# Kernel tuning notes

Measured on AMD Instinct MI355X. Metric: run time of the kernel, lower is better.

Reference implementation:

```python
import jax, jax.numpy as jnp
import numpy as np
import math

B, S, DIM, H, KVH = 2, 2048, 2048, 16, 4
HD = DIM // H          # 128
G = H // KVH           # 4 (GQA repeat factor)
NEG = -1e9             # fp32 additive mask value (matches torch path)


def _rotate_half(x):
    x1, x2 = jnp.split(x, 2, axis=-1)
    return jnp.concatenate([-x2, x1], axis=-1)


def setup_inputs() -> dict:
    key = jax.random.key(0)
    ks = jax.random.split(key, 8)
    hidden_states = jax.random.normal(ks[0], (B, S, DIM), jnp.float32)
    # standard RoPE tables [S, HD]
    inv_freq = 1.0 / (10000.0 ** (jnp.arange(0, HD, 2, dtype=jnp.float32) / HD))
    freqs = jnp.outer(jnp.arange(S, dtype=jnp.float32), inv_freq)
    emb = jnp.concatenate([freqs, freqs], axis=-1)
    position_cos = jnp.cos(emb)
    position_sin = jnp.sin(emb)
    alibi_bias = jax.random.normal(ks[1], (B, S, S), jnp.float32) * 0.01
    attention_mask = jnp.zeros((B, 1, 1, S), jnp.float32)
    sc = 0.02
    wq = jax.random.normal(ks[2], (DIM, DIM), jnp.float32) * sc
    wk = jax.random.normal(ks[3], (DIM, KVH * HD), jnp.float32) * sc
    wv = jax.random.normal(ks[4], (DIM, KVH * HD), jnp.float32) * sc
    wo = jax.random.normal(ks[5], (DIM, DIM), jnp.float32) * sc
    return {"hidden_states": hidden_states, "position_cos": position_cos,
            "position_sin": position_sin, "alibi_bias": alibi_bias,
            "attention_mask": attention_mask, "wq": wq, "wk": wk, "wv": wv, "wo": wo}


def reference(hidden_states, position_cos, position_sin, alibi_bias,
              attention_mask, wq, wk, wv, wo):
    b, s, d = hidden_states.shape
    # projections (weights stored as [in, out])
    q = (hidden_states @ wq).reshape(b, s, H, HD).transpose(0, 2, 1, 3)      # [B,H,S,HD]
    k = (hidden_states @ wk).reshape(b, s, KVH, HD).transpose(0, 2, 1, 3)    # [B,KVH,S,HD]
    v = (hidden_states @ wv).reshape(b, s, KVH, HD).transpose(0, 2, 1, 3)
    # RoPE
    cos = position_cos[None, None]  # [1,1,S,HD]
    sin = position_sin[None, None]
    q = q * cos + _rotate_half(q) * sin
    k = k * cos + _rotate_half(k) * sin
    # GQA repeat kv heads
    k = jnp.repeat(k, G, axis=1)   # [B,H,S,HD]
    v = jnp.repeat(v, G, axis=1)
    scores = jnp.einsum('bhqd,bhkd->bhqk', q, k) * (1.0 / math.sqrt(HD))
    causal = jnp.triu(jnp.full((s, s), NEG, jnp.float32), 1)
    scores = scores + causal + alibi_bias[:, None, :, :] + attention_mask
    attn = jax.nn.softmax(scores.astype(jnp.float32), axis=-1).astype(q.dtype)
    out = jnp.einsum('bhqk,bhkd->bhqd', attn, v)                              # [B,H,S,HD]
    out = out.transpose(0, 2, 1, 3).reshape(b, s, d)
    return out @ wo
```

## Files before the change

### kernel.cpp

```cpp
#include <hip/hip_runtime.h>
#include <hip/hip_bf16.h>

#define Bb   2
#define Ss   2048
#define Dd   2048
#define Hh   16
#define KVHh 4
#define HDd  128

typedef __bf16 bf16x8 __attribute__((ext_vector_type(8)));
typedef float f32x4 __attribute__((ext_vector_type(4)));

__device__ __forceinline__ unsigned short f2bf(float f) {
    unsigned u = __float_as_uint(f);
    unsigned r = (u + 0x7FFFu + ((u >> 16) & 1u)) >> 16;
    return (unsigned short)r;
}
__device__ __forceinline__ float bfu2f(unsigned short u) {
    return __uint_as_float(((unsigned)u) << 16);
}

#define GLOAD16(g, l) __builtin_amdgcn_global_load_lds( \
    (const __attribute__((address_space(1))) unsigned int*)(g), \
    (__attribute__((address_space(3))) unsigned int*)(l), 16, 0, 0)

__global__ __launch_bounds__(256)
void cast_bf16(const float* __restrict__ X, unsigned short* __restrict__ Y)
{
    int idx = blockIdx.x * 256 + threadIdx.x;
    float4 v = reinterpret_cast<const float4*>(X)[idx];
    ushort4 o;
    o.x = f2bf(v.x); o.y = f2bf(v.y); o.z = f2bf(v.z); o.w = f2bf(v.w);
    reinterpret_cast<ushort4*>(Y)[idx] = o;
}

__global__ __launch_bounds__(256)
void wt_cast(const float* __restrict__ W, unsigned short* __restrict__ WT,
             int K, int N)
{
    __shared__ float tile[32][33];
    int k0 = blockIdx.x * 32, n0 = blockIdx.y * 32;
    int tx = threadIdx.x & 31, ty = threadIdx.x >> 5;
    #pragma unroll
    for (int i = 0; i < 32; i += 8)
        tile[ty + i][tx] = W[(size_t)(k0 + ty + i) * N + n0 + tx];
    __syncthreads();
    #pragma unroll
    for (int i = 0; i < 32; i += 8)
        WT[(size_t)(n0 + ty + i) * K + k0 + tx] = f2bf(tile[tx][ty + i]);
}

template<bool BF16OUT>
__global__ __launch_bounds__(256)
void gemm_bt(const unsigned short* __restrict__ A,
             const unsigned short* __restrict__ BT,
             void* __restrict__ Cv, int M, int N, int K)
{
    __shared__ __align__(16) unsigned short sA[128 * 32];
    __shared__ __align__(16) unsigned short sB[128 * 32];
    const int tid  = threadIdx.x;
    const int wave = tid >> 6;
    const int lane = tid & 63;
    const int m    = lane & 15;
    const int quad = lane >> 4;
    const int wm   = wave >> 1, wn = wave & 1;
    const int m0   = blockIdx.y * 128, n0 = blockIdx.x * 128;

    const int srow = tid >> 2;
    const int skg  = (tid & 3) * 8;

    f32x4 acc[4][4];
    #pragma unroll
    for (int r = 0; r < 4; ++r)
        #pragma unroll
        for (int c = 0; c < 4; ++c) acc[r][c] = (f32x4){0.f, 0.f, 0.f, 0.f};

    const unsigned short* pa = A  + (size_t)(m0 + srow) * K + skg;
    const unsigned short* pb = BT + (size_t)(n0 + srow) * K + skg;
    unsigned short* la = &sA[wave * 16 * 32];
    unsigned short* lb = &sB[wave * 16 * 32];

    for (int k0 = 0; k0 < K; k0 += 32) {
        GLOAD16(pa + k0, la);
        GLOAD16(pa + (size_t)64 * K + k0, la + 64 * 32);
        GLOAD16(pb + k0, lb);
        GLOAD16(pb + (size_t)64 * K + k0, lb + 64 * 32);
        __syncthreads();
        bf16x8 af[4], bfr[4];
        #pragma unroll
        for (int r = 0; r < 4; ++r)
            af[r] = *reinterpret_cast<const bf16x8*>(
                &sA[(wm * 64 + r * 16 + m) * 32 + quad * 8]);
        #pragma unroll
        for (int c = 0; c < 4; ++c)
            bfr[c] = *reinterpret_cast<const bf16x8*>(
                &sB[(wn * 64 + c * 16 + m) * 32 + quad * 8]);
        #pragma unroll
        for (int r = 0; r < 4; ++r)
            #pragma unroll
            for (int c = 0; c < 4; ++c)
                acc[r][c] = __builtin_amdgcn_mfma_f32_16x16x32_bf16(
                    af[r], bfr[c], acc[r][c], 0, 0, 0);
        __syncthreads();
    }
    #pragma unroll
    for (int r = 0; r < 4; ++r)
        #pragma unroll
        for (int c = 0; c < 4; ++c)
            #pragma unroll
            for (int e = 0; e < 4; ++e) {
                size_t row = m0 + wm * 64 + r * 16 + quad * 4 + e;
                size_t col = n0 + wn * 64 + c * 16 + m;
                if (BF16OUT)
                    ((unsigned short*)Cv)[row * N + col] = f2bf(acc[r][c][e]);
                else
                    ((float*)Cv)[row * N + col] = acc[r][c][e];
            }
}

__global__ __launch_bounds__(256)
void rope_bf(unsigned short* __restrict__ X, const float* __restrict__ cosT,
             const float* __restrict__ sinT, int nhshift, int rowstride,
             float scale, int total)
{
    int idx = blockIdx.x * 256 + threadIdx.x;
    if (idx >= total) return;
    int i   = idx & 63;
    int rh  = idx >> 6;
    int row = rh >> nhshift;
    int h   = rh & ((1 << nhshift) - 1);
    int s   = row & (Ss - 1);
    unsigned short* xp = X + (size_t)row * rowstride + h * HDd;
    float x1 = bfu2f(xp[i]);
    float x2 = bfu2f(xp[i + 64]);
    float c1 = cosT[s * HDd + i];
    float c2 = cosT[s * HDd + i + 64];
    float s1 = sinT[s * HDd + i];
    float s2 = sinT[s * HDd + i + 64];
    xp[i]      = f2bf((x1 * c1 - x2 * s1) * scale);
    xp[i + 64] = f2bf((x2 * c2 + x1 * s2) * scale);
}

__global__ __launch_bounds__(256)
void vt_cast_bf(const unsigned short* __restrict__ KV,
                unsigned short* __restrict__ VT)
{
    __shared__ unsigned short tile[32][34];
    int st = blockIdx.x * 32, dt = blockIdx.y * 32;
    int bk = blockIdx.z;
    int b = bk >> 2, kvh = bk & 3;
    int tx = threadIdx.x & 31, ty = threadIdx.x >> 5;
    #pragma unroll
    for (int i = 0; i < 32; i += 8)
        tile[ty + i][tx] = KV[(size_t)(b * Ss + st + ty + i) * 1024 + 512 + kvh * HDd + dt + tx];
    __syncthreads();
    #pragma unroll
    for (int i = 0; i < 32; i += 8)
        VT[(((size_t)b * KVHh + kvh) * HDd + dt + ty + i) * Ss + st + tx] =
            tile[tx][ty + i];
}

__global__ __launch_bounds__(256, 2)
void flash_attn(const unsigned short* __restrict__ Qb,
                const unsigned short* __restrict__ KVb,
                const unsigned short* __restrict__ VT,
                const float* __restrict__ alibi,
                const float* __restrict__ amask,
                unsigned short* __restrict__ ctx)
{
    __shared__ __align__(16) unsigned short kbuf[2][32 * 128];
    __shared__ __align__(16) unsigned short vbuf[2][128 * 32];
    __shared__ unsigned short s_p[4][16][56];

    const int tid  = threadIdx.x;
    const int w    = tid >> 6;
    const int lane = tid & 63;
    const int m    = lane & 15;
    const int quad = lane >> 4;

    const int kvh = blockIdx.y;
    const int b   = blockIdx.z;
    const int h   = kvh * 4 + w;

    const unsigned short* vt0 = VT + ((size_t)b * KVHh + kvh) * HDd * Ss;
    const float* amrow = amask + (size_t)b * Ss;

    const int krow_s = tid >> 4;
    const int koff_b = ((tid & 15) * 16) ^ ((krow_s & 7) << 4);
    const int vrow_s = tid >> 2;
    const int vchk   = tid & 3;
    const int dstw   = w * 512;

    const unsigned short* kgbase = KVb + (size_t)b * Ss * 1024 + kvh * HDd;

    const int qts[2] = { (int)blockIdx.x, 127 - (int)blockIdx.x };

    #pragma unroll 1
    for (int pi = 0; pi < 2; ++pi) {
        const int q0 = qts[pi] * 16;

        bf16x8 qa[4];
        {
            const unsigned short* qrow = Qb + (size_t)(b * Ss + q0 + m) * Dd + h * HDd;
            #pragma unroll
            for (int c = 0; c < 4; ++c)
                qa[c] = *reinterpret_cast<const bf16x8*>(qrow + c * 32 + quad * 8);
        }

        f32x4 o[8];
        #pragma unroll
        for (int f = 0; f < 8; ++f) o[f] = (f32x4){0.f, 0.f, 0.f, 0.f};
        float lrow[4] = {0.f, 0.f, 0.f, 0.f};

        const float* arow = alibi + ((size_t)b * Ss + q0 + quad * 4) * Ss;
        const int ntiles = (q0 + 47) >> 5;

        {
            const unsigned short* kg = kgbase + (size_t)krow_s * 1024 + (koff_b >> 1);
            GLOAD16(kg,              &kbuf[0][dstw]);
            GLOAD16(kg + 16 * 1024,  &kbuf[0][2048 + dstw]);
            const unsigned short* vg = vt0 + (size_t)vrow_s * Ss + vchk * 8;
            GLOAD16(vg,              &vbuf[0][dstw]);
            GLOAD16(vg + 64 * Ss,    &vbuf[0][2048 + dstw]);
        }
        __syncthreads();

        #pragma unroll 1
        for (int kt = 0; kt < ntiles; ++kt) {
            const int k0  = kt * 32;
            const int cur = kt & 1;

            if (kt + 1 < ntiles) {
                const int kn = k0 + 32;
                const unsigned short* kg =
                    kgbase + (size_t)(kn + krow_s) * 1024 + (koff_b >> 1);
                GLOAD16(kg,              &kbuf[cur ^ 1][dstw]);
                GLOAD16(kg + 16 * 1024,  &kbuf[cur ^ 1][2048 + dstw]);
                const unsigned short* vg = vt0 + (size_t)vrow_s * Ss + kn + vchk * 8;
                GLOAD16(vg,              &vbuf[cur ^ 1][dstw]);
                GLOAD16(vg + 64 * Ss,    &vbuf[cur ^ 1][2048 + dstw]);
            }

            float al0[4], al1[4];
            #pragma unroll
            for (int r = 0; r < 4; ++r) {
                al0[r] = arow[(size_t)r * Ss + k0 + m];
                al1[r] = arow[(size_t)r * Ss + k0 + 16 + m];
            }
            const float am0 = amrow[k0 + m];
            const float am1 = amrow[k0 + 16 + m];

            const char* kb  = (const char*)&kbuf[cur][0];
            const char* vbp = (const char*)&vbuf[cur][0];
            const int  ksw  = (m & 7) << 4;
            bf16x8 kb0[4], kb1[4];
            #pragma unroll
            for (int c = 0; c < 4; ++c) {
                kb0[c] = *(const bf16x8*)(kb + m * 256        + ((c * 64 + quad * 16) ^ ksw));
                kb1[c] = *(const bf16x8*)(kb + (16 + m) * 256 + ((c * 64 + quad * 16) ^ ksw));
            }
            f32x4 s0 = {0.f, 0.f, 0.f, 0.f}, s1 = {0.f, 0.f, 0.f, 0.f};
            #pragma unroll
            for (int c = 0; c < 4; ++c) {
                s0 = __builtin_amdgcn_mfma_f32_16x16x32_bf16(qa[c], kb0[c], s0, 0, 0, 0);
                s1 = __builtin_amdgcn_mfma_f32_16x16x32_bf16(qa[c], kb1[c], s1, 0, 0, 0);
            }

            #pragma unroll
            for (int r = 0; r < 4; ++r) {
                const int qi = q0 + quad * 4 + r;
                float x0 = s0[r] + al0[r] + am0;
                float x1 = s1[r] + al1[r] + am1;
                x0 = (k0 + m      <= qi) ? x0 : -1e30f;
                x1 = (k0 + 16 + m <= qi) ? x1 : -1e30f;
                const float p0 = __expf(x0);
                const float p1 = __expf(x1);
                lrow[r] += p0 + p1;
                s_p[w][quad * 4 + r][m]      = f2bf(p0);
                s_p[w][quad * 4 + r][16 + m] = f2bf(p1);
            }
            __builtin_amdgcn_wave_barrier();
            const bf16x8 pa = *reinterpret_cast<const bf16x8*>(&s_p[w][m][quad * 8]);
            __builtin_amdgcn_wave_barrier();

            #pragma unroll
            for (int f = 0; f < 8; ++f) {
                const bf16x8 vb = *(const bf16x8*)(vbp + (f * 16 + m) * 64 + quad * 16);
                o[f] = __builtin_amdgcn_mfma_f32_16x16x32_bf16(pa, vb, o[f], 0, 0, 0);
            }

            __syncthreads();
        }

        float inv[4];
        #pragma unroll
        for (int r = 0; r < 4; ++r) {
            float l = lrow[r];
            l += __shfl_xor(l, 1, 64);
            l += __shfl_xor(l, 2, 64);
            l += __shfl_xor(l, 4, 64);
            l += __shfl_xor(l, 8, 64);
            inv[r] = 1.f / l;
        }
        #pragma unroll
        for (int f = 0; f < 8; ++f)
            #pragma unroll
            for (int r = 0; r < 4; ++r)
                ctx[(size_t)(b * Ss + q0 + quad * 4 + r) * Dd + h * HDd + f * 16 + m] =
                    f2bf(o[f][r] * inv[r]);
    }
}

extern "C" void kernel_launch(void* const* d_in, const int* in_sizes, int n_in,
                              void* d_out, int out_size, void* d_ws, size_t ws_size,
                              hipStream_t stream) {
    const float* hidden = (const float*)d_in[0];
    const float* cosT   = (const float*)d_in[1];
    const float* sinT   = (const float*)d_in[2];
    const float* alibi  = (const float*)d_in[3];
    const float* amask  = (const float*)d_in[4];
    const float* wq     = (const float*)d_in[5];
    const float* wk     = (const float*)d_in[6];
    const float* wv     = (const float*)d_in[7];
    const float* wo     = (const float*)d_in[8];
    float* out = (float*)d_out;

    char* ws = (char*)d_ws;
    unsigned short* Abf   = (unsigned short*)(ws);
    unsigned short* wqT   = (unsigned short*)(ws + 16777216);
    unsigned short* kvT   = (unsigned short*)(ws + 25165824);
    unsigned short* woT   = (unsigned short*)(ws + 29360128);
    unsigned short* Qraw  = (unsigned short*)(ws + 37748736);
    unsigned short* KVraw = (unsigned short*)(ws + 54525952);
    unsigned short* VT    = (unsigned short*)(ws + 62914560);
    unsigned short* Ctx   = (unsigned short*)(ws + 67108864);

    const int M = Bb * Ss;

    cast_bf16<<<(M * Dd / 4) / 256, 256, 0, stream>>>(hidden, Abf);
    wt_cast<<<dim3(64, 64), 256, 0, stream>>>(wq, wqT, Dd, Dd);
    wt_cast<<<dim3(64, 16), 256, 0, stream>>>(wk, kvT, Dd, 512);
    wt_cast<<<dim3(64, 16), 256, 0, stream>>>(wv, kvT + (size_t)512 * Dd, Dd, 512);
    wt_cast<<<dim3(64, 64), 256, 0, stream>>>(wo, woT, Dd, Dd);

    gemm_bt<true><<<dim3(Dd / 128, M / 128), 256, 0, stream>>>(Abf, wqT, Qraw, M, Dd, Dd);
    gemm_bt<true><<<dim3(1024 / 128, M / 128), 256, 0, stream>>>(Abf, kvT, KVraw, M, 1024, Dd);

    const float scale = 0.08838834764831845f;
    int totQ = Bb * Ss * Hh * 64;
    rope_bf<<<totQ / 256, 256, 0, stream>>>(Qraw, cosT, sinT, 4, Dd, scale, totQ);
    int totK = Bb * Ss * KVHh * 64;
    rope_bf<<<totK / 256, 256, 0, stream>>>(KVraw, cosT, sinT, 2, 1024, 1.0f, totK);

    vt_cast_bf<<<dim3(Ss / 32, HDd / 32, Bb * KVHh), 256, 0, stream>>>(KVraw, VT);

    flash_attn<<<dim3(64, KVHh, Bb), 256, 0, stream>>>(Qraw, KVraw, VT, alibi, amask, Ctx);

    gemm_bt<false><<<dim3(Dd / 128, M / 128), 256, 0, stream>>>(Ctx, woT, out, M, Dd, Dd);
}
```

Measured before the change: 433.7 us.

## Process 32 query rows per wave to reuse K/V tiles and prefetch alibi

Each block now handles one 32-row query tile per wave (two 16-row MFMA row blocks) instead of two 16-row tiles in sequence. Each K/V tile staged in LDS feeds twice as many rows, and per-row-block K/V loads and barriers are halved. Alibi bias, attention mask and causal masking are folded together and prefetched one tile ahead into double-buffered registers. The grid is remapped so batch and query-tile order come from blockIdx.x/z; register pressure from the doubled accumulators may reduce occupancy.

```diff
diff --git a/kernel.cpp b/kernel.cpp
--- a/kernel.cpp
+++ b/kernel.cpp
@@ -170,7 +170,7 @@
 {
     __shared__ __align__(16) unsigned short kbuf[2][32 * 128];
     __shared__ __align__(16) unsigned short vbuf[2][128 * 32];
-    __shared__ unsigned short s_p[4][16][56];
+    __shared__ unsigned short s_p[4][32][56];
 
     const int tid  = threadIdx.x;
     const int w    = tid >> 6;
@@ -178,12 +178,18 @@
     const int m    = lane & 15;
     const int quad = lane >> 4;
 
-    const int kvh = blockIdx.y;
-    const int b   = blockIdx.z;
-    const int h   = kvh * 4 + w;
+    const int pairIdx = blockIdx.x >> 1;
+    const int b       = blockIdx.x & 1;
+    const int kvh     = blockIdx.y;
+    const int qt      = blockIdx.z ? (63 - pairIdx) : pairIdx;
+    const int q0      = qt * 32;
+    const int ntiles  = qt + 1;
+    const int h       = kvh * 4 + w;
 
     const unsigned short* vt0 = VT + ((size_t)b * KVHh + kvh) * HDd * Ss;
     const float* amrow = amask + (size_t)b * Ss;
+    const float* arow  = alibi + ((size_t)b * Ss + q0) * Ss;
+    const unsigned short* kgbase = KVb + (size_t)b * Ss * 1024 + kvh * HDd;
 
     const int krow_s = tid >> 4;
     const int koff_b = ((tid & 15) * 16) ^ ((krow_s & 7) << 4);
@@ -191,124 +197,132 @@
     const int vchk   = tid & 3;
     const int dstw   = w * 512;
 
-    const unsigned short* kgbase = KVb + (size_t)b * Ss * 1024 + kvh * HDd;
-
-    const int qts[2] = { (int)blockIdx.x, 127 - (int)blockIdx.x };
-
-    #pragma unroll 1
-    for (int pi = 0; pi < 2; ++pi) {
-        const int q0 = qts[pi] * 16;
-
-        bf16x8 qa[4];
-        {
-            const unsigned short* qrow = Qb + (size_t)(b * Ss + q0 + m) * Dd + h * HDd;
+    bf16x8 qa[2][4];
+    #pragma unroll
+    for (int rb = 0; rb < 2; ++rb) {
+        const unsigned short* qrow =
+            Qb + (size_t)(b * Ss + q0 + rb * 16 + m) * Dd + h * HDd;
+        #pragma unroll
+        for (int c = 0; c < 4; ++c)
+            qa[rb][c] = *reinterpret_cast<const bf16x8*>(qrow + c * 32 + quad * 8);
+    }
+
+    f32x4 o[2][8];
+    #pragma unroll
+    for (int rb = 0; rb < 2; ++rb)
+        #pragma unroll
+        for (int f = 0; f < 8; ++f) o[rb][f] = (f32x4){0.f, 0.f, 0.f, 0.f};
+    float lrow[2][4] = {{0.f,0.f,0.f,0.f},{0.f,0.f,0.f,0.f}};
+
+    float alA[2][2][4], alB[2][2][4];
+
+    auto LDALIBI = [&](int k0n, float (&dst)[2][2][4]) {
+        const float am0 = amrow[k0n + m];
+        const float am1 = amrow[k0n + 16 + m];
+        #pragma unroll
+        for (int rb = 0; rb < 2; ++rb)
+            #pragma unroll
+            for (int r = 0; r < 4; ++r) {
+                const int row = rb * 16 + quad * 4 + r;
+                const int qi  = q0 + row;
+                const float* ap = arow + (size_t)row * Ss + k0n;
+                const float a0 = ap[m] + am0;
+                const float a1 = ap[16 + m] + am1;
+                dst[rb][0][r] = (k0n + m      <= qi) ? a0 : -1e30f;
+                dst[rb][1][r] = (k0n + 16 + m <= qi) ? a1 : -1e30f;
+            }
+    };
+
+    auto STAGE = [&](int kn, int buf) {
+        const unsigned short* kg = kgbase + (size_t)(kn + krow_s) * 1024 + (koff_b >> 1);
+        GLOAD16(kg,             &kbuf[buf][dstw]);
+        GLOAD16(kg + 16 * 1024, &kbuf[buf][2048 + dstw]);
+        const unsigned short* vg = vt0 + (size_t)vrow_s * Ss + kn + vchk * 8;
+        GLOAD16(vg,             &vbuf[buf][dstw]);
+        GLOAD16(vg + 64 * Ss,   &vbuf[buf][2048 + dstw]);
+    };
+
+    auto BODY = [&](int kt, float (&acur)[2][2][4], float (&anext)[2][2][4]) {
+        const int k0  = kt * 32;
+        const int cur = kt & 1;
+        if (kt + 1 < ntiles) {
+            STAGE(k0 + 32, cur ^ 1);
+            LDALIBI(k0 + 32, anext);
+        }
+        const char* kb  = (const char*)&kbuf[cur][0];
+        const int  ksw  = (m & 7) << 4;
+        bf16x8 kf[2][4];
+        #pragma unroll
+        for (int kh = 0; kh < 2; ++kh)
             #pragma unroll
             for (int c = 0; c < 4; ++c)
-                qa[c] = *reinterpret_cast<const bf16x8*>(qrow + c * 32 + quad * 8);
-        }
-
-        f32x4 o[8];
-        #pragma unroll
-        for (int f = 0; f < 8; ++f) o[f] = (f32x4){0.f, 0.f, 0.f, 0.f};
-        float lrow[4] = {0.f, 0.f, 0.f, 0.f};
-
-        const float* arow = alibi + ((size_t)b * Ss + q0 + quad * 4) * Ss;
-        const int ntiles = (q0 + 47) >> 5;
-
-        {
-            const unsigned short* kg = kgbase + (size_t)krow_s * 1024 + (koff_b >> 1);
-            GLOAD16(kg,              &kbuf[0][dstw]);
-            GLOAD16(kg + 16 * 1024,  &kbuf[0][2048 + dstw]);
-            const unsigned short* vg = vt0 + (size_t)vrow_s * Ss + vchk * 8;
-            GLOAD16(vg,              &vbuf[0][dstw]);
-            GLOAD16(vg + 64 * Ss,    &vbuf[0][2048 + dstw]);
+                kf[kh][c] = *(const bf16x8*)(kb + (kh * 16 + m) * 256 +
+                                             ((c * 64 + quad * 16) ^ ksw));
+        f32x4 s[2][2];
+        s[0][0] = (f32x4){0.f,0.f,0.f,0.f}; s[0][1] = (f32x4){0.f,0.f,0.f,0.f};
+        s[1][0] = (f32x4){0.f,0.f,0.f,0.f}; s[1][1] = (f32x4){0.f,0.f,0.f,0.f};
+        #pragma unroll
+        for (int c = 0; c < 4; ++c)
+            #pragma unroll
+            for (int rb = 0; rb < 2; ++rb)
+                #pragma unroll
+                for (int kh = 0; kh < 2; ++kh)
+                    s[rb][kh] = __builtin_amdgcn_mfma_f32_16x16x32_bf16(
+                        qa[rb][c], kf[kh][c], s[rb][kh], 0, 0, 0);
+        #pragma unroll
+        for (int rb = 0; rb < 2; ++rb)
+            #pragma unroll
+            for (int kh = 0; kh < 2; ++kh)
+                #pragma unroll
+                for (int r = 0; r < 4; ++r) {
+                    const float p = __expf(s[rb][kh][r] + acur[rb][kh][r]);
+                    lrow[rb][r] += p;
+                    s_p[w][rb * 16 + quad * 4 + r][kh * 16 + m] = f2bf(p);
+                }
+        __builtin_amdgcn_wave_barrier();
+        const bf16x8 pa0 = *reinterpret_cast<const bf16x8*>(&s_p[w][m][quad * 8]);
+        const bf16x8 pa1 = *reinterpret_cast<const bf16x8*>(&s_p[w][16 + m][quad * 8]);
+        __builtin_amdgcn_wave_barrier();
+        const char* vbp = (const char*)&vbuf[cur][0];
+        #pragma unroll
+        for (int f = 0; f < 8; ++f) {
+            const bf16x8 vb = *(const bf16x8*)(vbp + (f * 16 + m) * 64 + quad * 16);
+            o[0][f] = __builtin_amdgcn_mfma_f32_16x16x32_bf16(pa0, vb, o[0][f], 0, 0, 0);
+            o[1][f] = __builtin_amdgcn_mfma_f32_16x16x32_bf16(pa1, vb, o[1][f], 0, 0, 0);
         }
         __syncthreads();
-
-        #pragma unroll 1
-        for (int kt = 0; kt < ntiles; ++kt) {
-            const int k0  = kt * 32;
-            const int cur = kt & 1;
-
-            if (kt + 1 < ntiles) {
-                const int kn = k0 + 32;
-                const unsigned short* kg =
-                    kgbase + (size_t)(kn + krow_s) * 1024 + (koff_b >> 1);
-                GLOAD16(kg,              &kbuf[cur ^ 1][dstw]);
-                GLOAD16(kg + 16 * 1024,  &kbuf[cur ^ 1][2048 + dstw]);
-                const unsigned short* vg = vt0 + (size_t)vrow_s * Ss + kn + vchk * 8;
-                GLOAD16(vg,              &vbuf[cur ^ 1][dstw]);
-                GLOAD16(vg + 64 * Ss,    &vbuf[cur ^ 1][2048 + dstw]);
-            }
-
-            float al0[4], al1[4];
-            #pragma unroll
-            for (int r = 0; r < 4; ++r) {
-                al0[r] = arow[(size_t)r * Ss + k0 + m];
-                al1[r] = arow[(size_t)r * Ss + k0 + 16 + m];
-            }
-            const float am0 = amrow[k0 + m];
-            const float am1 = amrow[k0 + 16 + m];
-
-            const char* kb  = (const char*)&kbuf[cur][0];
-            const char* vbp = (const char*)&vbuf[cur][0];
-            const int  ksw  = (m & 7) << 4;
-            bf16x8 kb0[4], kb1[4];
-            #pragma unroll
-            for (int c = 0; c < 4; ++c) {
-                kb0[c] = *(const bf16x8*)(kb + m * 256        + ((c * 64 + quad * 16) ^ ksw));
-                kb1[c] = *(const bf16x8*)(kb + (16 + m) * 256 + ((c * 64 + quad * 16) ^ ksw));
-            }
-            f32x4 s0 = {0.f, 0.f, 0.f, 0.f}, s1 = {0.f, 0.f, 0.f, 0.f};
-            #pragma unroll
-            for (int c = 0; c < 4; ++c) {
-                s0 = __builtin_amdgcn_mfma_f32_16x16x32_bf16(qa[c], kb0[c], s0, 0, 0, 0);
-                s1 = __builtin_amdgcn_mfma_f32_16x16x32_bf16(qa[c], kb1[c], s1, 0, 0, 0);
-            }
-
-            #pragma unroll
-            for (int r = 0; r < 4; ++r) {
-                const int qi = q0 + quad * 4 + r;
-                float x0 = s0[r] + al0[r] + am0;
-                float x1 = s1[r] + al1[r] + am1;
-                x0 = (k0 + m      <= qi) ? x0 : -1e30f;
-                x1 = (k0 + 16 + m <= qi) ? x1 : -1e30f;
-                const float p0 = __expf(x0);
-                const float p1 = __expf(x1);
-                lrow[r] += p0 + p1;
-                s_p[w][quad * 4 + r][m]      = f2bf(p0);
-                s_p[w][quad * 4 + r][16 + m] = f2bf(p1);
-            }
-            __builtin_amdgcn_wave_barrier();
-            const bf16x8 pa = *reinterpret_cast<const bf16x8*>(&s_p[w][m][quad * 8]);
-            __builtin_amdgcn_wave_barrier();
-
-            #pragma unroll
-            for (int f = 0; f < 8; ++f) {
-                const bf16x8 vb = *(const bf16x8*)(vbp + (f * 16 + m) * 64 + quad * 16);
-                o[f] = __builtin_amdgcn_mfma_f32_16x16x32_bf16(pa, vb, o[f], 0, 0, 0);
-            }
-
-            __syncthreads();
-        }
-
-        float inv[4];
+    };
+
+    LDALIBI(0, alA);
+    STAGE(0, 0);
+    __syncthreads();
+
+    int kt = 0;
+    while (true) {
+        BODY(kt, alA, alB); if (++kt >= ntiles) break;
+        BODY(kt, alB, alA); if (++kt >= ntiles) break;
+    }
+
+    float inv[2][4];
+    #pragma unroll
+    for (int rb = 0; rb < 2; ++rb)
         #pragma unroll
         for (int r = 0; r < 4; ++r) {
-            float l = lrow[r];
+            float l = lrow[rb][r];
             l += __shfl_xor(l, 1, 64);
             l += __shfl_xor(l, 2, 64);
             l += __shfl_xor(l, 4, 64);
             l += __shfl_xor(l, 8, 64);
-            inv[r] = 1.f / l;
+            inv[rb][r] = 1.f / l;
         }
+    #pragma unroll
+    for (int rb = 0; rb < 2; ++rb)
         #pragma unroll
         for (int f = 0; f < 8; ++f)
             #pragma unroll
             for (int r = 0; r < 4; ++r)
-                ctx[(size_t)(b * Ss + q0 + quad * 4 + r) * Dd + h * HDd + f * 16 + m] =
-                    f2bf(o[f][r] * inv[r]);
-    }
+                ctx[(size_t)(b * Ss + q0 + rb * 16 + quad * 4 + r) * Dd +
+                    h * HDd + f * 16 + m] = f2bf(o[rb][f][r] * inv[rb][r]);
 }
 
 extern "C" void kernel_launch(void* const* d_in, const int* in_sizes, int n_in,
@@ -354,7 +368,7 @@
 
     vt_cast_bf<<<dim3(Ss / 32, HDd / 32, Bb * KVHh), 256, 0, stream>>>(KVraw, VT);
 
-    flash_attn<<<dim3(64, KVHh, Bb), 256, 0, stream>>>(Qraw, KVraw, VT, alibi, amask, Ctx);
+    flash_attn<<<dim3(64, KVHh, 2), 256, 0, stream>>>(Qraw, KVraw, VT, alibi, amask, Ctx);
 
     gemm_bt<false><<<dim3(Dd / 128, M / 128), 256, 0, stream>>>(Ctx, woT, out, M, Dd, Dd);
 }
```

Result: slower. 478.1 us (+10.2%).
